# Kernel tuning notes

Hardware: AMD Instinct MI355X
Metric: run time of the kernel (lower is better)

## Reference

```python
import jax, jax.numpy as jnp
import numpy as np
import math

BS, S, D = 2, 2048, 2048
DOWN, UP, H, RD = 512, 1024, 16, 32
HD = D // H            # 128, used only in softmax scale
VD = UP // H           # 64 per-head value dim
CD = UP // H           # 64 per-head content q/k dim
SCALE = math.sqrt(HD) + math.sqrt(RD)


def _rope(x, head_dim):
    # x: [bs, heads, seq, head_dim]; standard rotate-half RoPE
    seq = x.shape[2]
    inv_freq = 1.0 / (10000.0 ** (jnp.arange(0, head_dim, 2, dtype=jnp.float32) / head_dim))
    freqs = jnp.arange(seq, dtype=jnp.float32)[:, None] * inv_freq[None, :]  # [S, hd/2]
    emb = jnp.concatenate([freqs, freqs], axis=-1)                            # [S, hd]
    cos = jnp.cos(emb)[None, None]
    sin = jnp.sin(emb)[None, None]
    x1, x2 = x[..., : head_dim // 2], x[..., head_dim // 2 :]
    rot = jnp.concatenate([-x2, x1], axis=-1)
    return x * cos + rot * sin


def setup_inputs() -> dict:
    key = jax.random.key(0)
    ks = jax.random.split(key, 10)
    sd = 0.02
    inp = {
        'h': jax.random.normal(ks[0], (BS, S, D), jnp.float32),
        'mask': jnp.tril(jnp.ones((1, 1, S, S), jnp.int32)),
        'Wdkv': jax.random.normal(ks[1], (DOWN, D), jnp.float32) * sd,
        'bdkv': jnp.zeros((DOWN,), jnp.float32),
        'Wuk': jax.random.normal(ks[2], (UP, DOWN), jnp.float32) * sd,
        'buk': jnp.zeros((UP,), jnp.float32),
        'Wuv': jax.random.normal(ks[3], (UP, DOWN), jnp.float32) * sd,
        'buv': jnp.zeros((UP,), jnp.float32),
        'Wdq': jax.random.normal(ks[4], (DOWN, D), jnp.float32) * sd,
        'bdq': jnp.zeros((DOWN,), jnp.float32),
        'Wuq': jax.random.normal(ks[5], (UP, DOWN), jnp.float32) * sd,
        'buq': jnp.zeros((UP,), jnp.float32),
        'Wqr': jax.random.normal(ks[6], (RD * H, DOWN), jnp.float32) * sd,
        'bqr': jnp.zeros((RD * H,), jnp.float32),
        'Wkr': jax.random.normal(ks[7], (RD, D), jnp.float32) * sd,
        'bkr': jnp.zeros((RD,), jnp.float32),
        'Wfc': jax.random.normal(ks[8], (D, H * VD), jnp.float32) * sd,
        'bfc': jnp.zeros((D,), jnp.float32),
    }
    return inp


def reference(h, mask, Wdkv, bdkv, Wuk, buk, Wuv, buv, Wdq, bdq, Wuq, buq,
              Wqr, bqr, Wkr, bkr, Wfc, bfc):
    bs, seq, _ = h.shape
    # low-rank KV path
    c_kv = h @ Wdkv.T + bdkv                                   # [bs,S,DOWN]
    k_c = (c_kv @ Wuk.T + buk).reshape(bs, seq, H, CD).transpose(0, 2, 1, 3)
    v_c = (c_kv @ Wuv.T + buv).reshape(bs, seq, H, VD).transpose(0, 2, 1, 3)
    # low-rank Q path
    c_q = h @ Wdq.T + bdq                                      # [bs,S,DOWN]
    q_c = (c_q @ Wuq.T + buq).reshape(bs, seq, H, CD).transpose(0, 2, 1, 3)
    # decoupled RoPE paths
    q_r = _rope((c_q @ Wqr.T + bqr).reshape(bs, seq, H, RD).transpose(0, 2, 1, 3), RD)
    k_r = _rope((h @ Wkr.T + bkr).reshape(bs, seq, 1, RD).transpose(0, 2, 1, 3), RD)
    k_r = jnp.broadcast_to(k_r, (bs, H, seq, RD))              # shared RoPE key across heads
    q = jnp.concatenate([q_c, q_r], axis=-1)                   # [bs,H,S,CD+RD]
    k = jnp.concatenate([k_c, k_r], axis=-1)
    scores = jnp.einsum('bhqd,bhkd->bhqk', q, k)
    # NB: original applies mask BEFORE dividing by scale
    scores = jnp.where(mask == 0, -1e9, scores)
    probs = jax.nn.softmax(scores / SCALE, axis=-1)
    out = jnp.einsum('bhqk,bhkd->bhqd', probs, v_c)            # [bs,H,S,VD]
    out = out.transpose(0, 2, 1, 3).reshape(bs, seq, H * VD)
    return out @ Wfc.T + bfc
```

## Files before the change

### kernel.cpp

```cpp
#include <hip/hip_runtime.h>
#include <hip/hip_bf16.h>
#include <math.h>

typedef unsigned short u16;
typedef __attribute__((ext_vector_type(8))) short bf16x8;
typedef __attribute__((ext_vector_type(4))) float f32x4;
typedef __attribute__((ext_vector_type(16))) float f32x16;

namespace {

constexpr int BS = 2;
constexpr int S = 2048;
constexpr int D = 2048;
constexpr int DOWN = 512;
constexpr int UP = 1024;
constexpr int H = 16;
constexpr int RD = 32;
constexpr int VD = 64;
constexpr int QKD = 96;
constexpr int M = BS * S;
constexpr int N1 = 1152;
constexpr int N2 = 2048;
constexpr int N3 = 1536;

__device__ __forceinline__ float b2f(u16 u) {
  unsigned int x = ((unsigned int)u) << 16;
  return __uint_as_float(x);
}
__device__ __forceinline__ u16 f2b(float f) {
  unsigned int u = __float_as_uint(f);
  u += 0x7fff + ((u >> 16) & 1);
  return (u16)(u >> 16);
}
__device__ __forceinline__ void store_out(float* p, float v) { *p = v; }
__device__ __forceinline__ void store_out(u16* p, float v) { *p = f2b(v); }

__device__ __forceinline__ void async16(const u16* g, u16* lds) {
  __builtin_amdgcn_global_load_lds(
      (const __attribute__((address_space(1))) unsigned int*)g,
      (__attribute__((address_space(3))) unsigned int*)lds, 16, 0, 0);
}

__device__ __forceinline__ float exp2_fast(float x) {
#if __has_builtin(__builtin_amdgcn_exp2f)
  return __builtin_amdgcn_exp2f(x);
#else
  float r;
  asm("v_exp_f32 %0, %1" : "=v"(r) : "v"(x));
  return r;
#endif
}

__device__ __forceinline__ unsigned pkbf(float a, float b) {
  union { __hip_bfloat162 h; unsigned u; } c;
  c.h = __float22bfloat162_rn(make_float2(a, b));
  return c.u;
}
__device__ __forceinline__ void plswap(unsigned& a, unsigned& b) {
  asm("v_permlane32_swap_b32 %0, %1" : "+v"(a), "+v"(b));
}

__device__ __forceinline__ f32x4 mfma32(bf16x8 a, bf16x8 b, f32x4 c) {
  return __builtin_amdgcn_mfma_f32_16x16x32_bf16(a, b, c, 0, 0, 0);
}
__device__ __forceinline__ f32x16 mfma3216(bf16x8 a, bf16x8 b, f32x16 c) {
  return __builtin_amdgcn_mfma_f32_32x32x16_bf16(a, b, c, 0, 0, 0);
}

__global__ __launch_bounds__(256) void prep_kernel(
    const float* __restrict__ h, const float* __restrict__ Wdkv,
    const float* __restrict__ Wdq, const float* __restrict__ Wkr,
    const float* __restrict__ Wuk, const float* __restrict__ Wuv,
    const float* __restrict__ Wuq, const float* __restrict__ Wqr,
    const float* __restrict__ Wfc, const float* __restrict__ bdkv,
    const float* __restrict__ bdq, const float* __restrict__ bkr,
    const float* __restrict__ buk, const float* __restrict__ buv,
    const float* __restrict__ buq, const float* __restrict__ bqr,
    u16* __restrict__ hb, u16* __restrict__ Wcat1, u16* __restrict__ Wcat2,
    u16* __restrict__ Wcat3, u16* __restrict__ Wfcb,
    float* __restrict__ bcat1, float* __restrict__ bcat2,
    float* __restrict__ bcat3, float* __restrict__ ct, float* __restrict__ st) {
  const long i = (long)blockIdx.x * 256 + threadIdx.x;
  if (i >= 3630240) return;
  if (i < 3620864) {
    const float* src; u16* dst; long off;
    if      (i < 2097152) { src = h;    dst = hb;              off = i; }
    else if (i < 2359296) { src = Wdkv; dst = Wcat1;           off = i - 2097152; }
    else if (i < 2621440) { src = Wdq;  dst = Wcat1 + 1048576; off = i - 2359296; }
    else if (i < 2637824) { src = Wkr;  dst = Wcat1 + 2097152; off = i - 2621440; }
    else if (i < 2768896) { src = Wuk;  dst = Wcat2;           off = i - 2637824; }
    else if (i < 2899968) { src = Wuv;  dst = Wcat2 + 524288;  off = i - 2768896; }
    else if (i < 3031040) { src = Wuq;  dst = Wcat3;           off = i - 2899968; }
    else if (i < 3096576) { src = Wqr;  dst = Wcat3 + 524288;  off = i - 3031040; }
    else                  { src = Wfc;  dst = Wfcb;            off = i - 3096576; }
    float4 v = ((const float4*)src)[off];
    ushort4 o;
    o.x = f2b(v.x); o.y = f2b(v.y); o.z = f2b(v.z); o.w = f2b(v.w);
    ((ushort4*)dst)[off] = o;
  } else if (i < 3622048) {
    long j0 = (i - 3620864) * 4;
#pragma unroll
    for (int e = 0; e < 4; ++e) {
      long j = j0 + e;
      if (j < N1) {
        float v = 0.f;
        if (j < 512) v = bdkv[j];
        else if (j < 1024) v = bdq[j - 512];
        else if (j < 1056) v = bkr[j - 1024];
        bcat1[j] = v;
      } else if (j < N1 + N2) {
        long jj = j - N1;
        bcat2[jj] = (jj < 1024) ? buk[jj] : buv[jj - 1024];
      } else {
        long jj = j - N1 - N2;
        bcat3[jj] = (jj < 1024) ? buq[jj] : bqr[jj - 1024];
      }
    }
  } else {
    long k0 = (i - 3622048) * 4;
#pragma unroll
    for (int e = 0; e < 4; ++e) {
      long k = k0 + e;
      int s = (int)(k >> 4), r = (int)(k & 15);
      float f = powf(10000.f, -(float)r / 16.f);
      float th = (float)s * f;
      ct[k] = cosf(th);
      st[k] = sinf(th);
    }
  }
}

template <int BN, typename OutT>
__device__ __forceinline__ void gemm_body(
    const u16* __restrict__ A, int lda, const u16* __restrict__ W, int ldw,
    const float* __restrict__ bias, OutT* __restrict__ C, int ldc, int K,
    int m0, int n0) {
  constexpr int NFR = BN / 32;
  __shared__ u16 As[128 * 32];
  __shared__ u16 Bs[BN * 32];
  const int t = threadIdx.x;
  const int lane = t & 63, wave = t >> 6;
  const int wm = (wave >> 1) * 64, wn = (wave & 1) * (BN / 2);
  const int lrow = lane & 15, lk = (lane >> 4) * 8;
  const int srow = lane >> 2, scol = (lane & 3) * 8;
  f32x4 acc[4][NFR] = {};
  for (int k0 = 0; k0 < K; k0 += 32) {
    __syncthreads();
    {
      int r = wave * 32 + srow;
      async16(A + (size_t)(m0 + r) * lda + k0 + scol, As + (wave * 32) * 32);
      async16(A + (size_t)(m0 + r + 16) * lda + k0 + scol,
              As + (wave * 32 + 16) * 32);
    }
    if (BN == 128) {
      int r = wave * 32 + srow;
      async16(W + (size_t)(n0 + r) * ldw + k0 + scol, Bs + (wave * 32) * 32);
      async16(W + (size_t)(n0 + r + 16) * ldw + k0 + scol,
              Bs + (wave * 32 + 16) * 32);
    } else {
      int r = wave * 16 + srow;
      async16(W + (size_t)(n0 + r) * ldw + k0 + scol, Bs + (wave * 16) * 32);
    }
    __syncthreads();
    bf16x8 af[4], bfr[NFR];
#pragma unroll
    for (int i = 0; i < 4; ++i)
      af[i] = *(const bf16x8*)(As + (wm + i * 16 + lrow) * 32 + lk);
#pragma unroll
    for (int i = 0; i < NFR; ++i)
      bfr[i] = *(const bf16x8*)(Bs + (wn + i * 16 + lrow) * 32 + lk);
#pragma unroll
    for (int mi = 0; mi < 4; ++mi)
#pragma unroll
      for (int ni = 0; ni < NFR; ++ni)
        acc[mi][ni] = mfma32(af[mi], bfr[ni], acc[mi][ni]);
  }
#pragma unroll
  for (int mi = 0; mi < 4; ++mi)
#pragma unroll
    for (int ni = 0; ni < NFR; ++ni)
#pragma unroll
      for (int r = 0; r < 4; ++r) {
        int m = m0 + wm + mi * 16 + (lane >> 4) * 4 + r;
        int n = n0 + wn + ni * 16 + lrow;
        store_out(C + (size_t)m * ldc + n, acc[mi][ni][r] + bias[n]);
      }
}

template <int BN, typename OutT>
__global__ __launch_bounds__(256) void gemm_bt_mfma(
    const u16* __restrict__ A, int lda, const u16* __restrict__ W, int ldw,
    const float* __restrict__ bias, OutT* __restrict__ C, int ldc, int K) {
  gemm_body<BN, OutT>(A, lda, W, ldw, bias, C, ldc, K,
                      blockIdx.x * 128, blockIdx.y * BN);
}

__global__ __launch_bounds__(256) void gemm_up_fused(
    const u16* __restrict__ C1v, const u16* __restrict__ Wcat2,
    const u16* __restrict__ Wcat3, const float* __restrict__ bcat2,
    const float* __restrict__ bcat3, u16* __restrict__ C2,
    u16* __restrict__ C3) {
  const int by = blockIdx.y;
  const u16* A;
  const u16* W;
  const float* bias;
  u16* C;
  int ldc, n0;
  if (by < 16) {
    A = C1v; W = Wcat2; bias = bcat2; C = C2; ldc = N2; n0 = by * 128;
  } else {
    A = C1v + DOWN; W = Wcat3; bias = bcat3; C = C3; ldc = N3;
    n0 = (by - 16) * 128;
  }
  gemm_body<128, u16>(A, N1, W, DOWN, bias, C, ldc, DOWN,
                      blockIdx.x * 128, n0);
}

__global__ __launch_bounds__(256) void transpose_v_kernel(
    const u16* __restrict__ in, int ld_in, u16* __restrict__ VtB) {
  __shared__ u16 tile[64][72];
  const int m0 = blockIdx.x * 64;
  const int h = blockIdx.y;
  const int r = threadIdx.x >> 2, c0 = (threadIdx.x & 3) * 16;
  *(bf16x8*)(&tile[r][c0]) =
      *(const bf16x8*)(in + (size_t)(m0 + r) * ld_in + h * VD + c0);
  *(bf16x8*)(&tile[r][c0 + 8]) =
      *(const bf16x8*)(in + (size_t)(m0 + r) * ld_in + h * VD + c0 + 8);
  __syncthreads();
  bf16x8 o0, o1;
#pragma unroll
  for (int j = 0; j < 8; ++j) {
    o0[j] = (short)tile[c0 + j][r];
    o1[j] = (short)tile[c0 + 8 + j][r];
  }
  const int b = m0 / S, sb = m0 % S;
  size_t dst = ((size_t)(b * H + h) * 64 + ((sb + c0) >> 5)) * 2048 +
               (size_t)r * 32 + ((sb + c0) & 31);
  *(bf16x8*)(VtB + dst) = o0;
  *(bf16x8*)(VtB + dst + 8) = o1;
}

__global__ __launch_bounds__(192) void pack_q_kernel(
    const u16* __restrict__ qc, const u16* __restrict__ qr,
    const float* __restrict__ ct, const float* __restrict__ st,
    u16* __restrict__ Qp) {
  const int t = threadIdx.x;
  const int sub = (t >= 96) ? 1 : 0;
  const int d = t - sub * 96;
  const int s = blockIdx.x * 2 + sub, h = blockIdx.y, b = blockIdx.z;
  const float sc = 1.44269504088896f / (sqrtf(128.f) + sqrtf(32.f));
  float val;
  if (d < 64) {
    val = b2f(qc[(size_t)(b * S + s) * N3 + h * VD + d]);
  } else {
    int r = d - 64;
    const u16* qrow = qr + (size_t)(b * S + s) * N3 + h * RD;
    float x = b2f(qrow[r]), xp = b2f(qrow[r ^ 16]);
    float c = ct[s * 16 + (r & 15)], sn = st[s * 16 + (r & 15)];
    val = (r < 16) ? (x * c - xp * sn) : (x * c + xp * sn);
  }
  Qp[((size_t)(b * H + h) * S + s) * QKD + d] = f2b(val * sc);
}

__global__ __launch_bounds__(192) void pack_k_kernel(
    const u16* __restrict__ kc,
    const u16* __restrict__ kr,
    const float* __restrict__ ct, const float* __restrict__ st,
    u16* __restrict__ Kp) {
  const int t = threadIdx.x;
  const int sub = (t >= 96) ? 1 : 0;
  const int d = t - sub * 96;
  const int s = blockIdx.x * 2 + sub, h = blockIdx.y, b = blockIdx.z;
  float val;
  if (d < 64) {
    val = b2f(kc[(size_t)(b * S + s) * N2 + h * VD + d]);
  } else {
    int r = d - 64;
    const u16* krow = kr + (size_t)(b * S + s) * N1;
    float x = b2f(krow[r]), xp = b2f(krow[r ^ 16]);
    float c = ct[s * 16 + (r & 15)], sn = st[s * 16 + (r & 15)];
    val = (r < 16) ? (x * c - xp * sn) : (x * c + xp * sn);
  }
  Kp[((size_t)(b * H + h) * S + s) * QKD + d] = f2b(val);
}

__global__ __launch_bounds__(256, 3) void attn_mfma(
    const u16* __restrict__ Qp, const u16* __restrict__ Kp,
    const u16* __restrict__ Vt, u16* __restrict__ attnb) {
  const int t = threadIdx.x, wave = t >> 6, lane = t & 63;
  const int l31 = lane & 31, hw = lane >> 5;
  const int bh = blockIdx.x & 31;
  const int b = bh >> 4, h = bh & 15;
  const int tile = 63 - (blockIdx.x >> 5);
  const int q0w = tile * 32;
  const size_t hbo = (size_t)bh * S;

  __shared__ float red[3][64][33];

  bf16x8 qf[6];
  {
    const u16* qrow = Qp + (hbo + q0w + l31) * QKD + hw * 8;
#pragma unroll
    for (int c = 0; c < 6; ++c) qf[c] = *(const bf16x8*)(qrow + c * 16);
  }
  f32x16 O0 = {0,0,0,0,0,0,0,0,0,0,0,0,0,0,0,0};
  f32x16 O1 = {0,0,0,0,0,0,0,0,0,0,0,0,0,0,0,0};
  float lsum = 0.f;
  const int q_abs = q0w + l31;
  const u16* vbase = Vt + (size_t)bh * 64 * 2048 + l31 * 32 + 8 * hw;

  bf16x8 kf[6];
  {
    const u16* kb = Kp + (hbo + wave * 32 + l31) * QKD + hw * 8;
#pragma unroll
    for (int c = 0; c < 6; ++c) kf[c] = *(const bf16x8*)(kb + c * 16);
  }

  for (int m = wave; m <= tile; m += 4) {
    const int k0 = m * 32;
    const u16* vb = vbase + (size_t)m * 2048;
    bf16x8 vf00 = *(const bf16x8*)(vb);
    bf16x8 vf01 = *(const bf16x8*)(vb + 16);
    bf16x8 vf10 = *(const bf16x8*)(vb + 1024);
    bf16x8 vf11 = *(const bf16x8*)(vb + 1024 + 16);
    f32x16 sa = {0,0,0,0,0,0,0,0,0,0,0,0,0,0,0,0};
    f32x16 sb = {0,0,0,0,0,0,0,0,0,0,0,0,0,0,0,0};
    sa = mfma3216(kf[0], qf[0], sa);
    sb = mfma3216(kf[1], qf[1], sb);
    sa = mfma3216(kf[2], qf[2], sa);
    sb = mfma3216(kf[3], qf[3], sb);
    sa = mfma3216(kf[4], qf[4], sa);
    sb = mfma3216(kf[5], qf[5], sb);
    if (m + 4 <= tile) {
      const u16* kb = Kp + (hbo + (size_t)(m + 4) * 32 + l31) * QKD + hw * 8;
#pragma unroll
      for (int c = 0; c < 6; ++c) kf[c] = *(const bf16x8*)(kb + c * 16);
    }
    float e[16];
    if (m == tile) {
#pragma unroll
      for (int r = 0; r < 16; ++r) {
        int key_abs = k0 + (r & 3) + 8 * (r >> 2) + 4 * hw;
        float v = exp2_fast(sa[r] + sb[r]);
        e[r] = (key_abs <= q_abs) ? v : 0.f;
      }
    } else {
#pragma unroll
      for (int r = 0; r < 16; ++r) e[r] = exp2_fast(sa[r] + sb[r]);
    }
    {
      float p0 = (e[0] + e[1]) + (e[2] + e[3]);
      float p1 = (e[4] + e[5]) + (e[6] + e[7]);
      float p2 = (e[8] + e[9]) + (e[10] + e[11]);
      float p3 = (e[12] + e[13]) + (e[14] + e[15]);
      lsum += (p0 + p1) + (p2 + p3);
    }
    unsigned w0 = pkbf(e[0], e[1]),   w1 = pkbf(e[2], e[3]);
    unsigned w2 = pkbf(e[4], e[5]),   w3 = pkbf(e[6], e[7]);
    unsigned w4 = pkbf(e[8], e[9]),   w5 = pkbf(e[10], e[11]);
    unsigned w6 = pkbf(e[12], e[13]), w7 = pkbf(e[14], e[15]);
    plswap(w0, w2); plswap(w1, w3); plswap(w4, w6); plswap(w5, w7);
    union { unsigned u[4]; bf16x8 v; } ua, ub;
    ua.u[0] = w0; ua.u[1] = w1; ua.u[2] = w2; ua.u[3] = w3;
    ub.u[0] = w4; ub.u[1] = w5; ub.u[2] = w6; ub.u[3] = w7;
    O0 = mfma3216(ua.v, vf00, O0);
    O1 = mfma3216(ua.v, vf10, O1);
    O0 = mfma3216(ub.v, vf01, O0);
    O1 = mfma3216(ub.v, vf11, O1);
  }

  if (wave > 0) {
#pragma unroll
    for (int r = 0; r < 16; ++r) {
      red[wave - 1][lane][r] = O0[r];
      red[wave - 1][lane][16 + r] = O1[r];
    }
    red[wave - 1][lane][32] = lsum;
  }
  __syncthreads();
  if (wave == 0) {
#pragma unroll
    for (int w = 0; w < 3; ++w) {
#pragma unroll
      for (int r = 0; r < 16; ++r) {
        O0[r] += red[w][lane][r];
        O1[r] += red[w][lane][16 + r];
      }
      lsum += red[w][lane][32];
    }
    float tot = lsum + __shfl_xor(lsum, 32);
    u16* ob = attnb + (size_t)b * S * UP + h * VD;
#pragma unroll
    for (int r = 0; r < 16; ++r) {
      int rowq = (r & 3) + 8 * (r >> 2) + 4 * hw;
      float linv = 1.f / __shfl(tot, rowq);
      size_t rowoff = (size_t)(q0w + rowq) * UP;
      ob[rowoff + l31] = f2b(O0[r] * linv);
      ob[rowoff + 32 + l31] = f2b(O1[r] * linv);
    }
  }
}

}

extern "C" void kernel_launch(void* const* d_in, const int* in_sizes, int n_in,
                              void* d_out, int out_size, void* d_ws, size_t ws_size,
                              hipStream_t stream) {
  const float* h    = (const float*)d_in[0];
  const float* Wdkv = (const float*)d_in[2];
  const float* bdkv = (const float*)d_in[3];
  const float* Wuk  = (const float*)d_in[4];
  const float* buk  = (const float*)d_in[5];
  const float* Wuv  = (const float*)d_in[6];
  const float* buv  = (const float*)d_in[7];
  const float* Wdq  = (const float*)d_in[8];
  const float* bdq  = (const float*)d_in[9];
  const float* Wuq  = (const float*)d_in[10];
  const float* buq  = (const float*)d_in[11];
  const float* Wqr  = (const float*)d_in[12];
  const float* bqr  = (const float*)d_in[13];
  const float* Wkr  = (const float*)d_in[14];
  const float* bkr  = (const float*)d_in[15];
  const float* Wfc  = (const float*)d_in[16];
  const float* bfc  = (const float*)d_in[17];
  float* out = (float*)d_out;

  u16* p = (u16*)d_ws;
  u16* hb    = p; p += (size_t)M * D;
  u16* Wcat1 = p; p += (size_t)N1 * D;
  u16* Wcat2 = p; p += (size_t)N2 * DOWN;
  u16* Wcat3 = p; p += (size_t)N3 * DOWN;
  u16* Wfcb  = p; p += (size_t)D * UP;
  u16* C1    = p; p += (size_t)M * N1;
  u16* C2    = p; p += (size_t)M * N2;
  u16* C3    = p; p += (size_t)M * N3;
  u16* Qp    = p; p += 6291456;
  u16* Kp    = p; p += 6291456;
  u16* Vt    = p; p += (size_t)UP * M;
  float* bcat1 = (float*)p; p += 2 * N1;
  float* bcat2 = (float*)p; p += 2 * N2;
  float* bcat3 = (float*)p; p += 2 * N3;
  float* ct = (float*)p; p += 2 * S * 16;
  float* st = (float*)p; p += 2 * S * 16;
  u16* attnb = C1;

  prep_kernel<<<dim3(14181), 256, 0, stream>>>(
      h, Wdkv, Wdq, Wkr, Wuk, Wuv, Wuq, Wqr, Wfc,
      bdkv, bdq, bkr, buk, buv, buq, bqr,
      hb, Wcat1, Wcat2, Wcat3, Wfcb, bcat1, bcat2, bcat3, ct, st);

  gemm_bt_mfma<64, u16><<<dim3(M / 128, N1 / 64), 256, 0, stream>>>(
      hb, D, Wcat1, D, bcat1, C1, N1, D);
  gemm_up_fused<<<dim3(M / 128, 28), 256, 0, stream>>>(
      C1, Wcat2, Wcat3, bcat2, bcat3, C2, C3);

  pack_q_kernel<<<dim3(S / 2, H, BS), 192, 0, stream>>>(
      C3, C3 + UP, ct, st, Qp);
  pack_k_kernel<<<dim3(S / 2, H, BS), 192, 0, stream>>>(
      C2, C1 + 2 * DOWN, ct, st, Kp);
  transpose_v_kernel<<<dim3(M / 64, UP / 64), 256, 0, stream>>>(
      C2 + UP, N2, Vt);

  attn_mfma<<<dim3(2048), 256, 0, stream>>>(Qp, Kp, Vt, attnb);

  gemm_bt_mfma<64, float><<<dim3(M / 128, D / 64), 256, 0, stream>>>(
      attnb, UP, Wfcb, UP, bfc, out, D, UP);
}
```

Before: 318.3 us.

## Pair causal attention tiles per block, double-buffer K/V loads, widen GEMM tiles

The attention kernel now handles two query tiles per block (tile 63-tp and tp), so every block does a similar amount of causal work. The grid shrinks to 1024 blocks and the launch-bound occupancy drops from 3 to 2. K and V fragments are prefetched into ping-pong register buffers so the V loads also overlap compute. Separately, the first projection GEMM and the output GEMM switch to 128-wide N tiles, which halves their grid size. This raises register pressure and reduces the number of blocks, which risks lower occupancy and tail effects.

```diff
diff --git a/kernel.cpp b/kernel.cpp
--- a/kernel.cpp
+++ b/kernel.cpp
@@ -284,120 +284,152 @@
   Kp[((size_t)(b * H + h) * S + s) * QKD + d] = f2b(val);
 }
 
-__global__ __launch_bounds__(256, 3) void attn_mfma(
+__global__ __launch_bounds__(256, 2) void attn_mfma(
     const u16* __restrict__ Qp, const u16* __restrict__ Kp,
     const u16* __restrict__ Vt, u16* __restrict__ attnb) {
   const int t = threadIdx.x, wave = t >> 6, lane = t & 63;
   const int l31 = lane & 31, hw = lane >> 5;
   const int bh = blockIdx.x & 31;
   const int b = bh >> 4, h = bh & 15;
-  const int tile = 63 - (blockIdx.x >> 5);
-  const int q0w = tile * 32;
+  const int tp = blockIdx.x >> 5;
   const size_t hbo = (size_t)bh * S;
+  const u16* vbase = Vt + (size_t)bh * 64 * 2048 + l31 * 32 + 8 * hw;
 
   __shared__ float red[3][64][33];
 
-  bf16x8 qf[6];
-  {
-    const u16* qrow = Qp + (hbo + q0w + l31) * QKD + hw * 8;
-#pragma unroll
-    for (int c = 0; c < 6; ++c) qf[c] = *(const bf16x8*)(qrow + c * 16);
-  }
-  f32x16 O0 = {0,0,0,0,0,0,0,0,0,0,0,0,0,0,0,0};
-  f32x16 O1 = {0,0,0,0,0,0,0,0,0,0,0,0,0,0,0,0};
-  float lsum = 0.f;
-  const int q_abs = q0w + l31;
-  const u16* vbase = Vt + (size_t)bh * 64 * 2048 + l31 * 32 + 8 * hw;
-
-  bf16x8 kf[6];
-  {
-    const u16* kb = Kp + (hbo + wave * 32 + l31) * QKD + hw * 8;
-#pragma unroll
-    for (int c = 0; c < 6; ++c) kf[c] = *(const bf16x8*)(kb + c * 16);
-  }
-
-  for (int m = wave; m <= tile; m += 4) {
-    const int k0 = m * 32;
-    const u16* vb = vbase + (size_t)m * 2048;
-    bf16x8 vf00 = *(const bf16x8*)(vb);
-    bf16x8 vf01 = *(const bf16x8*)(vb + 16);
-    bf16x8 vf10 = *(const bf16x8*)(vb + 1024);
-    bf16x8 vf11 = *(const bf16x8*)(vb + 1024 + 16);
-    f32x16 sa = {0,0,0,0,0,0,0,0,0,0,0,0,0,0,0,0};
-    f32x16 sb = {0,0,0,0,0,0,0,0,0,0,0,0,0,0,0,0};
-    sa = mfma3216(kf[0], qf[0], sa);
-    sb = mfma3216(kf[1], qf[1], sb);
-    sa = mfma3216(kf[2], qf[2], sa);
-    sb = mfma3216(kf[3], qf[3], sb);
-    sa = mfma3216(kf[4], qf[4], sa);
-    sb = mfma3216(kf[5], qf[5], sb);
-    if (m + 4 <= tile) {
-      const u16* kb = Kp + (hbo + (size_t)(m + 4) * 32 + l31) * QKD + hw * 8;
-#pragma unroll
-      for (int c = 0; c < 6; ++c) kf[c] = *(const bf16x8*)(kb + c * 16);
-    }
-    float e[16];
-    if (m == tile) {
+#pragma unroll 1
+  for (int pass = 0; pass < 2; ++pass) {
+    const int tile = pass ? tp : 63 - tp;
+    const int q0w = tile * 32;
+    const int q_abs = q0w + l31;
+
+    bf16x8 qf[6];
+    {
+      const u16* qrow = Qp + (hbo + q0w + l31) * QKD + hw * 8;
+#pragma unroll
+      for (int c = 0; c < 6; ++c) qf[c] = *(const bf16x8*)(qrow + c * 16);
+    }
+    f32x16 O0 = {0,0,0,0,0,0,0,0,0,0,0,0,0,0,0,0};
+    f32x16 O1 = {0,0,0,0,0,0,0,0,0,0,0,0,0,0,0,0};
+    float lsum = 0.f;
+
+    auto step = [&](const bf16x8* kf, const bf16x8* vf, int m) {
+      f32x16 sa = {0,0,0,0,0,0,0,0,0,0,0,0,0,0,0,0};
+      f32x16 sb = {0,0,0,0,0,0,0,0,0,0,0,0,0,0,0,0};
+      sa = mfma3216(kf[0], qf[0], sa);
+      sb = mfma3216(kf[1], qf[1], sb);
+      sa = mfma3216(kf[2], qf[2], sa);
+      sb = mfma3216(kf[3], qf[3], sb);
+      sa = mfma3216(kf[4], qf[4], sa);
+      sb = mfma3216(kf[5], qf[5], sb);
+      float e[16];
+      if (m == tile) {
+        const int k0 = m * 32;
+#pragma unroll
+        for (int r = 0; r < 16; ++r) {
+          int key_abs = k0 + (r & 3) + 8 * (r >> 2) + 4 * hw;
+          float v = exp2_fast(sa[r] + sb[r]);
+          e[r] = (key_abs <= q_abs) ? v : 0.f;
+        }
+      } else {
+#pragma unroll
+        for (int r = 0; r < 16; ++r) e[r] = exp2_fast(sa[r] + sb[r]);
+      }
+      {
+        float p0 = (e[0] + e[1]) + (e[2] + e[3]);
+        float p1 = (e[4] + e[5]) + (e[6] + e[7]);
+        float p2 = (e[8] + e[9]) + (e[10] + e[11]);
+        float p3 = (e[12] + e[13]) + (e[14] + e[15]);
+        lsum += (p0 + p1) + (p2 + p3);
+      }
+      unsigned w0 = pkbf(e[0], e[1]),   w1 = pkbf(e[2], e[3]);
+      unsigned w2 = pkbf(e[4], e[5]),   w3 = pkbf(e[6], e[7]);
+      unsigned w4 = pkbf(e[8], e[9]),   w5 = pkbf(e[10], e[11]);
+      unsigned w6 = pkbf(e[12], e[13]), w7 = pkbf(e[14], e[15]);
+      plswap(w0, w2); plswap(w1, w3); plswap(w4, w6); plswap(w5, w7);
+      union { unsigned u[4]; bf16x8 v; } ua, ub;
+      ua.u[0] = w0; ua.u[1] = w1; ua.u[2] = w2; ua.u[3] = w3;
+      ub.u[0] = w4; ub.u[1] = w5; ub.u[2] = w6; ub.u[3] = w7;
+      O0 = mfma3216(ua.v, vf[0], O0);
+      O1 = mfma3216(ua.v, vf[2], O1);
+      O0 = mfma3216(ub.v, vf[1], O0);
+      O1 = mfma3216(ub.v, vf[3], O1);
+    };
+
+    if (tile >= wave) {
+      bf16x8 kfE[6], kfO[6], vfE[4], vfO[4];
+      int m = wave;
+      {
+        const u16* kb = Kp + (hbo + (size_t)m * 32 + l31) * QKD + hw * 8;
+#pragma unroll
+        for (int c = 0; c < 6; ++c) kfE[c] = *(const bf16x8*)(kb + c * 16);
+        const u16* vb = vbase + (size_t)m * 2048;
+        vfE[0] = *(const bf16x8*)(vb);
+        vfE[1] = *(const bf16x8*)(vb + 16);
+        vfE[2] = *(const bf16x8*)(vb + 1024);
+        vfE[3] = *(const bf16x8*)(vb + 1024 + 16);
+      }
+      while (true) {
+        if (m + 4 <= tile) {
+          const u16* kb = Kp + (hbo + (size_t)(m + 4) * 32 + l31) * QKD + hw * 8;
+#pragma unroll
+          for (int c = 0; c < 6; ++c) kfO[c] = *(const bf16x8*)(kb + c * 16);
+          const u16* vb = vbase + (size_t)(m + 4) * 2048;
+          vfO[0] = *(const bf16x8*)(vb);
+          vfO[1] = *(const bf16x8*)(vb + 16);
+          vfO[2] = *(const bf16x8*)(vb + 1024);
+          vfO[3] = *(const bf16x8*)(vb + 1024 + 16);
+        }
+        step(kfE, vfE, m);
+        m += 4;
+        if (m > tile) break;
+        if (m + 4 <= tile) {
+          const u16* kb = Kp + (hbo + (size_t)(m + 4) * 32 + l31) * QKD + hw * 8;
+#pragma unroll
+          for (int c = 0; c < 6; ++c) kfE[c] = *(const bf16x8*)(kb + c * 16);
+          const u16* vb = vbase + (size_t)(m + 4) * 2048;
+          vfE[0] = *(const bf16x8*)(vb);
+          vfE[1] = *(const bf16x8*)(vb + 16);
+          vfE[2] = *(const bf16x8*)(vb + 1024);
+          vfE[3] = *(const bf16x8*)(vb + 1024 + 16);
+        }
+        step(kfO, vfO, m);
+        m += 4;
+        if (m > tile) break;
+      }
+    }
+
+    if (wave > 0) {
 #pragma unroll
       for (int r = 0; r < 16; ++r) {
-        int key_abs = k0 + (r & 3) + 8 * (r >> 2) + 4 * hw;
-        float v = exp2_fast(sa[r] + sb[r]);
-        e[r] = (key_abs <= q_abs) ? v : 0.f;
-      }
-    } else {
-#pragma unroll
-      for (int r = 0; r < 16; ++r) e[r] = exp2_fast(sa[r] + sb[r]);
-    }
-    {
-      float p0 = (e[0] + e[1]) + (e[2] + e[3]);
-      float p1 = (e[4] + e[5]) + (e[6] + e[7]);
-      float p2 = (e[8] + e[9]) + (e[10] + e[11]);
-      float p3 = (e[12] + e[13]) + (e[14] + e[15]);
-      lsum += (p0 + p1) + (p2 + p3);
-    }
-    unsigned w0 = pkbf(e[0], e[1]),   w1 = pkbf(e[2], e[3]);
-    unsigned w2 = pkbf(e[4], e[5]),   w3 = pkbf(e[6], e[7]);
-    unsigned w4 = pkbf(e[8], e[9]),   w5 = pkbf(e[10], e[11]);
-    unsigned w6 = pkbf(e[12], e[13]), w7 = pkbf(e[14], e[15]);
-    plswap(w0, w2); plswap(w1, w3); plswap(w4, w6); plswap(w5, w7);
-    union { unsigned u[4]; bf16x8 v; } ua, ub;
-    ua.u[0] = w0; ua.u[1] = w1; ua.u[2] = w2; ua.u[3] = w3;
-    ub.u[0] = w4; ub.u[1] = w5; ub.u[2] = w6; ub.u[3] = w7;
-    O0 = mfma3216(ua.v, vf00, O0);
-    O1 = mfma3216(ua.v, vf10, O1);
-    O0 = mfma3216(ub.v, vf01, O0);
-    O1 = mfma3216(ub.v, vf11, O1);
-  }
-
-  if (wave > 0) {
-#pragma unroll
-    for (int r = 0; r < 16; ++r) {
-      red[wave - 1][lane][r] = O0[r];
-      red[wave - 1][lane][16 + r] = O1[r];
-    }
-    red[wave - 1][lane][32] = lsum;
-  }
-  __syncthreads();
-  if (wave == 0) {
-#pragma unroll
-    for (int w = 0; w < 3; ++w) {
+        red[wave - 1][lane][r] = O0[r];
+        red[wave - 1][lane][16 + r] = O1[r];
+      }
+      red[wave - 1][lane][32] = lsum;
+    }
+    __syncthreads();
+    if (wave == 0) {
+#pragma unroll
+      for (int w = 0; w < 3; ++w) {
+#pragma unroll
+        for (int r = 0; r < 16; ++r) {
+          O0[r] += red[w][lane][r];
+          O1[r] += red[w][lane][16 + r];
+        }
+        lsum += red[w][lane][32];
+      }
+      float tot = lsum + __shfl_xor(lsum, 32);
+      u16* ob = attnb + (size_t)b * S * UP + h * VD;
 #pragma unroll
       for (int r = 0; r < 16; ++r) {
-        O0[r] += red[w][lane][r];
-        O1[r] += red[w][lane][16 + r];
-      }
-      lsum += red[w][lane][32];
-    }
-    float tot = lsum + __shfl_xor(lsum, 32);
-    u16* ob = attnb + (size_t)b * S * UP + h * VD;
-#pragma unroll
-    for (int r = 0; r < 16; ++r) {
-      int rowq = (r & 3) + 8 * (r >> 2) + 4 * hw;
-      float linv = 1.f / __shfl(tot, rowq);
-      size_t rowoff = (size_t)(q0w + rowq) * UP;
-      ob[rowoff + l31] = f2b(O0[r] * linv);
-      ob[rowoff + 32 + l31] = f2b(O1[r] * linv);
-    }
+        int rowq = (r & 3) + 8 * (r >> 2) + 4 * hw;
+        float linv = 1.f / __shfl(tot, rowq);
+        size_t rowoff = (size_t)(q0w + rowq) * UP;
+        ob[rowoff + l31] = f2b(O0[r] * linv);
+        ob[rowoff + 32 + l31] = f2b(O1[r] * linv);
+      }
+    }
+    __syncthreads();
   }
 }
 
@@ -449,7 +481,7 @@
       bdkv, bdq, bkr, buk, buv, buq, bqr,
       hb, Wcat1, Wcat2, Wcat3, Wfcb, bcat1, bcat2, bcat3, ct, st);
 
-  gemm_bt_mfma<64, u16><<<dim3(M / 128, N1 / 64), 256, 0, stream>>>(
+  gemm_bt_mfma<128, u16><<<dim3(M / 128, N1 / 128), 256, 0, stream>>>(
       hb, D, Wcat1, D, bcat1, C1, N1, D);
   gemm_up_fused<<<dim3(M / 128, 28), 256, 0, stream>>>(
       C1, Wcat2, Wcat3, bcat2, bcat3, C2, C3);
@@ -461,8 +493,8 @@
   transpose_v_kernel<<<dim3(M / 64, UP / 64), 256, 0, stream>>>(
       C2 + UP, N2, Vt);
 
-  attn_mfma<<<dim3(2048), 256, 0, stream>>>(Qp, Kp, Vt, attnb);
-
-  gemm_bt_mfma<64, float><<<dim3(M / 128, D / 64), 256, 0, stream>>>(
+  attn_mfma<<<dim3(1024), 256, 0, stream>>>(Qp, Kp, Vt, attnb);
+
+  gemm_bt_mfma<128, float><<<dim3(M / 128, D / 128), 256, 0, stream>>>(
       attnb, UP, Wfcb, UP, bfc, out, D, UP);
 }
```

Measured after the change: 325.6 us. 1.02x slower.

## Restructure attention to share LDS-staged K/V tiles across waves; widen GEMM tiles

Applied to the files above, without the earlier changes.

The attention kernel previously split one 32-query tile's key loop across four waves and combined their partial results through shared memory. Now each block covers four consecutive query tiles, one per wave. K and V chunks are staged into double-buffered LDS with async copies and shared by all waves, and the cross-wave reduction is removed. This cuts redundant global K/V loads, at the cost of a barrier every iteration, load imbalance across waves near the causal diagonal, and fewer blocks (512). The two plain GEMM launches also move from 64 to 128 N-tiles, which halves their grid sizes.

```diff
diff --git a/kernel.cpp b/kernel.cpp
--- a/kernel.cpp
+++ b/kernel.cpp
@@ -284,18 +284,26 @@
   Kp[((size_t)(b * H + h) * S + s) * QKD + d] = f2b(val);
 }
 
-__global__ __launch_bounds__(256, 3) void attn_mfma(
+__global__ __launch_bounds__(256, 2) void attn_mfma(
     const u16* __restrict__ Qp, const u16* __restrict__ Kp,
     const u16* __restrict__ Vt, u16* __restrict__ attnb) {
   const int t = threadIdx.x, wave = t >> 6, lane = t & 63;
   const int l31 = lane & 31, hw = lane >> 5;
   const int bh = blockIdx.x & 31;
   const int b = bh >> 4, h = bh & 15;
-  const int tile = 63 - (blockIdx.x >> 5);
-  const int q0w = tile * 32;
+  const int qq = 15 - (int)(blockIdx.x >> 5);
+  const int mtop = qq * 4 + 3;
+  const int tw = qq * 4 + wave;
+  const int q0w = tw * 32;
   const size_t hbo = (size_t)bh * S;
 
-  __shared__ float red[3][64][33];
+  __shared__ u16 KsB[2][3072];
+  __shared__ u16 VsB[2][2048];
+
+  const u16* kpb = Kp + hbo * QKD;
+  const int ksrc = l31 * QKD + hw * 8;
+  const u16* vtb = Vt + (size_t)bh * 64 * 2048;
+  const int vsrc = lane * 32;
 
   bf16x8 qf[6];
   {
@@ -307,97 +315,89 @@
   f32x16 O1 = {0,0,0,0,0,0,0,0,0,0,0,0,0,0,0,0};
   float lsum = 0.f;
   const int q_abs = q0w + l31;
-  const u16* vbase = Vt + (size_t)bh * 64 * 2048 + l31 * 32 + 8 * hw;
-
-  bf16x8 kf[6];
-  {
-    const u16* kb = Kp + (hbo + wave * 32 + l31) * QKD + hw * 8;
-#pragma unroll
-    for (int c = 0; c < 6; ++c) kf[c] = *(const bf16x8*)(kb + c * 16);
-  }
-
-  for (int m = wave; m <= tile; m += 4) {
-    const int k0 = m * 32;
-    const u16* vb = vbase + (size_t)m * 2048;
-    bf16x8 vf00 = *(const bf16x8*)(vb);
-    bf16x8 vf01 = *(const bf16x8*)(vb + 16);
-    bf16x8 vf10 = *(const bf16x8*)(vb + 1024);
-    bf16x8 vf11 = *(const bf16x8*)(vb + 1024 + 16);
-    f32x16 sa = {0,0,0,0,0,0,0,0,0,0,0,0,0,0,0,0};
-    f32x16 sb = {0,0,0,0,0,0,0,0,0,0,0,0,0,0,0,0};
-    sa = mfma3216(kf[0], qf[0], sa);
-    sb = mfma3216(kf[1], qf[1], sb);
-    sa = mfma3216(kf[2], qf[2], sa);
-    sb = mfma3216(kf[3], qf[3], sb);
-    sa = mfma3216(kf[4], qf[4], sa);
-    sb = mfma3216(kf[5], qf[5], sb);
-    if (m + 4 <= tile) {
-      const u16* kb = Kp + (hbo + (size_t)(m + 4) * 32 + l31) * QKD + hw * 8;
-#pragma unroll
-      for (int c = 0; c < 6; ++c) kf[c] = *(const bf16x8*)(kb + c * 16);
-    }
-    float e[16];
-    if (m == tile) {
-#pragma unroll
-      for (int r = 0; r < 16; ++r) {
-        int key_abs = k0 + (r & 3) + 8 * (r >> 2) + 4 * hw;
-        float v = exp2_fast(sa[r] + sb[r]);
-        e[r] = (key_abs <= q_abs) ? v : 0.f;
+
+  auto stage = [&](int buf, int m) {
+    const u16* kr = kpb + (size_t)m * 32 * QKD + ksrc;
+    const u16* vr = vtb + (size_t)m * 2048 + vsrc;
+    u16* ks = &KsB[buf][0];
+    u16* vs = &VsB[buf][0];
+    for (int idx = wave; idx < 10; idx += 4) {
+      if (idx < 6) {
+        async16(kr + idx * 16, ks + idx * 512);
+      } else {
+        int j = idx - 6;
+        async16(vr + (j >> 1) * 16 + (j & 1) * 8, vs + j * 512);
       }
-    } else {
-#pragma unroll
-      for (int r = 0; r < 16; ++r) e[r] = exp2_fast(sa[r] + sb[r]);
-    }
-    {
-      float p0 = (e[0] + e[1]) + (e[2] + e[3]);
-      float p1 = (e[4] + e[5]) + (e[6] + e[7]);
-      float p2 = (e[8] + e[9]) + (e[10] + e[11]);
-      float p3 = (e[12] + e[13]) + (e[14] + e[15]);
-      lsum += (p0 + p1) + (p2 + p3);
-    }
-    unsigned w0 = pkbf(e[0], e[1]),   w1 = pkbf(e[2], e[3]);
-    unsigned w2 = pkbf(e[4], e[5]),   w3 = pkbf(e[6], e[7]);
-    unsigned w4 = pkbf(e[8], e[9]),   w5 = pkbf(e[10], e[11]);
-    unsigned w6 = pkbf(e[12], e[13]), w7 = pkbf(e[14], e[15]);
-    plswap(w0, w2); plswap(w1, w3); plswap(w4, w6); plswap(w5, w7);
-    union { unsigned u[4]; bf16x8 v; } ua, ub;
-    ua.u[0] = w0; ua.u[1] = w1; ua.u[2] = w2; ua.u[3] = w3;
-    ub.u[0] = w4; ub.u[1] = w5; ub.u[2] = w6; ub.u[3] = w7;
-    O0 = mfma3216(ua.v, vf00, O0);
-    O1 = mfma3216(ua.v, vf10, O1);
-    O0 = mfma3216(ub.v, vf01, O0);
-    O1 = mfma3216(ub.v, vf11, O1);
-  }
-
-  if (wave > 0) {
-#pragma unroll
-    for (int r = 0; r < 16; ++r) {
-      red[wave - 1][lane][r] = O0[r];
-      red[wave - 1][lane][16 + r] = O1[r];
-    }
-    red[wave - 1][lane][32] = lsum;
-  }
+    }
+  };
+
+  stage(0, 0);
   __syncthreads();
-  if (wave == 0) {
-#pragma unroll
-    for (int w = 0; w < 3; ++w) {
-#pragma unroll
-      for (int r = 0; r < 16; ++r) {
-        O0[r] += red[w][lane][r];
-        O1[r] += red[w][lane][16 + r];
+  for (int m = 0; m <= mtop; ++m) {
+    if (m < mtop) stage((m + 1) & 1, m + 1);
+    if (m <= tw) {
+      const u16* ks = &KsB[m & 1][lane * 8];
+      const u16* vs = &VsB[m & 1][hw * 512 + l31 * 8];
+      bf16x8 kf[6];
+#pragma unroll
+      for (int c = 0; c < 6; ++c) kf[c] = *(const bf16x8*)(ks + c * 512);
+      f32x16 sa = {0,0,0,0,0,0,0,0,0,0,0,0,0,0,0,0};
+      f32x16 sb = {0,0,0,0,0,0,0,0,0,0,0,0,0,0,0,0};
+      sa = mfma3216(kf[0], qf[0], sa);
+      sb = mfma3216(kf[1], qf[1], sb);
+      sa = mfma3216(kf[2], qf[2], sa);
+      sb = mfma3216(kf[3], qf[3], sb);
+      sa = mfma3216(kf[4], qf[4], sa);
+      sb = mfma3216(kf[5], qf[5], sb);
+      float e[16];
+      if (m == tw) {
+        const int k0 = m * 32;
+#pragma unroll
+        for (int r = 0; r < 16; ++r) {
+          int key_abs = k0 + (r & 3) + 8 * (r >> 2) + 4 * hw;
+          float v = exp2_fast(sa[r] + sb[r]);
+          e[r] = (key_abs <= q_abs) ? v : 0.f;
+        }
+      } else {
+#pragma unroll
+        for (int r = 0; r < 16; ++r) e[r] = exp2_fast(sa[r] + sb[r]);
       }
-      lsum += red[w][lane][32];
-    }
-    float tot = lsum + __shfl_xor(lsum, 32);
-    u16* ob = attnb + (size_t)b * S * UP + h * VD;
-#pragma unroll
-    for (int r = 0; r < 16; ++r) {
-      int rowq = (r & 3) + 8 * (r >> 2) + 4 * hw;
-      float linv = 1.f / __shfl(tot, rowq);
-      size_t rowoff = (size_t)(q0w + rowq) * UP;
-      ob[rowoff + l31] = f2b(O0[r] * linv);
-      ob[rowoff + 32 + l31] = f2b(O1[r] * linv);
-    }
+      {
+        float p0 = (e[0] + e[1]) + (e[2] + e[3]);
+        float p1 = (e[4] + e[5]) + (e[6] + e[7]);
+        float p2 = (e[8] + e[9]) + (e[10] + e[11]);
+        float p3 = (e[12] + e[13]) + (e[14] + e[15]);
+        lsum += (p0 + p1) + (p2 + p3);
+      }
+      unsigned w0 = pkbf(e[0], e[1]),   w1 = pkbf(e[2], e[3]);
+      unsigned w2 = pkbf(e[4], e[5]),   w3 = pkbf(e[6], e[7]);
+      unsigned w4 = pkbf(e[8], e[9]),   w5 = pkbf(e[10], e[11]);
+      unsigned w6 = pkbf(e[12], e[13]), w7 = pkbf(e[14], e[15]);
+      plswap(w0, w2); plswap(w1, w3); plswap(w4, w6); plswap(w5, w7);
+      union { unsigned u[4]; bf16x8 v; } ua, ub;
+      ua.u[0] = w0; ua.u[1] = w1; ua.u[2] = w2; ua.u[3] = w3;
+      ub.u[0] = w4; ub.u[1] = w5; ub.u[2] = w6; ub.u[3] = w7;
+      bf16x8 vf00 = *(const bf16x8*)(vs);
+      bf16x8 vf10 = *(const bf16x8*)(vs + 256);
+      bf16x8 vf01 = *(const bf16x8*)(vs + 1024);
+      bf16x8 vf11 = *(const bf16x8*)(vs + 1280);
+      O0 = mfma3216(ua.v, vf00, O0);
+      O1 = mfma3216(ua.v, vf10, O1);
+      O0 = mfma3216(ub.v, vf01, O0);
+      O1 = mfma3216(ub.v, vf11, O1);
+    }
+    __syncthreads();
+  }
+
+  float tot = lsum + __shfl_xor(lsum, 32);
+  u16* ob = attnb + (size_t)b * S * UP + h * VD;
+#pragma unroll
+  for (int r = 0; r < 16; ++r) {
+    int rowq = (r & 3) + 8 * (r >> 2) + 4 * hw;
+    float linv = 1.f / __shfl(tot, rowq);
+    size_t rowoff = (size_t)(q0w + rowq) * UP;
+    ob[rowoff + l31] = f2b(O0[r] * linv);
+    ob[rowoff + 32 + l31] = f2b(O1[r] * linv);
   }
 }
 
@@ -449,7 +449,7 @@
       bdkv, bdq, bkr, buk, buv, buq, bqr,
       hb, Wcat1, Wcat2, Wcat3, Wfcb, bcat1, bcat2, bcat3, ct, st);
 
-  gemm_bt_mfma<64, u16><<<dim3(M / 128, N1 / 64), 256, 0, stream>>>(
+  gemm_bt_mfma<128, u16><<<dim3(M / 128, N1 / 128), 256, 0, stream>>>(
       hb, D, Wcat1, D, bcat1, C1, N1, D);
   gemm_up_fused<<<dim3(M / 128, 28), 256, 0, stream>>>(
       C1, Wcat2, Wcat3, bcat2, bcat3, C2, C3);
@@ -461,8 +461,8 @@
   transpose_v_kernel<<<dim3(M / 64, UP / 64), 256, 0, stream>>>(
       C2 + UP, N2, Vt);
 
-  attn_mfma<<<dim3(2048), 256, 0, stream>>>(Qp, Kp, Vt, attnb);
-
-  gemm_bt_mfma<64, float><<<dim3(M / 128, D / 64), 256, 0, stream>>>(
+  attn_mfma<<<dim3(512), 256, 0, stream>>>(Qp, Kp, Vt, attnb);
+
+  gemm_bt_mfma<128, float><<<dim3(M / 128, D / 128), 256, 0, stream>>>(
       attnb, UP, Wfcb, UP, bfc, out, D, UP);
 }
```

Result: slower. 334.9 us (+5.2%).

## Double-buffer V loads in attention, remap blocks per XCD, widen GEMM tiles

Applied to the files above, without the earlier changes.

The attention loop now prefetches the next V tile into alternating register buffers alongside the K prefetch, so the loads overlap the current tile's MFMA and softmax work. Blocks are remapped so that each XCD handles a fixed group of four (batch, head) pairs, which should improve L2 reuse of K and V. The first and last GEMMs switch from 64-wide to 128-wide N tiles, halving their grid sizes. The added register buffers raise register pressure and could reduce occupancy, and the wider GEMM tiles leave fewer blocks to spread across the CUs.

```diff
diff --git a/kernel.cpp b/kernel.cpp
--- a/kernel.cpp
+++ b/kernel.cpp
@@ -289,9 +289,10 @@
     const u16* __restrict__ Vt, u16* __restrict__ attnb) {
   const int t = threadIdx.x, wave = t >> 6, lane = t & 63;
   const int l31 = lane & 31, hw = lane >> 5;
-  const int bh = blockIdx.x & 31;
+  const int xcd = (int)(blockIdx.x & 7), sub = (int)(blockIdx.x >> 3);
+  const int bh = xcd * 4 + (sub & 3);
+  const int tile = 63 - (sub >> 2);
   const int b = bh >> 4, h = bh & 15;
-  const int tile = 63 - (blockIdx.x >> 5);
   const int q0w = tile * 32;
   const size_t hbo = (size_t)bh * S;
 
@@ -308,36 +309,21 @@
   float lsum = 0.f;
   const int q_abs = q0w + l31;
   const u16* vbase = Vt + (size_t)bh * 64 * 2048 + l31 * 32 + 8 * hw;
-
-  bf16x8 kf[6];
-  {
-    const u16* kb = Kp + (hbo + wave * 32 + l31) * QKD + hw * 8;
-#pragma unroll
-    for (int c = 0; c < 6; ++c) kf[c] = *(const bf16x8*)(kb + c * 16);
-  }
-
-  for (int m = wave; m <= tile; m += 4) {
-    const int k0 = m * 32;
-    const u16* vb = vbase + (size_t)m * 2048;
-    bf16x8 vf00 = *(const bf16x8*)(vb);
-    bf16x8 vf01 = *(const bf16x8*)(vb + 16);
-    bf16x8 vf10 = *(const bf16x8*)(vb + 1024);
-    bf16x8 vf11 = *(const bf16x8*)(vb + 1024 + 16);
-    f32x16 sa = {0,0,0,0,0,0,0,0,0,0,0,0,0,0,0,0};
-    f32x16 sb = {0,0,0,0,0,0,0,0,0,0,0,0,0,0,0,0};
+  const u16* kpb = Kp + hbo * QKD;
+
+  auto qk_part1 = [&](bf16x8* kf, f32x16& sa, f32x16& sb) {
     sa = mfma3216(kf[0], qf[0], sa);
     sb = mfma3216(kf[1], qf[1], sb);
     sa = mfma3216(kf[2], qf[2], sa);
     sb = mfma3216(kf[3], qf[3], sb);
     sa = mfma3216(kf[4], qf[4], sa);
     sb = mfma3216(kf[5], qf[5], sb);
-    if (m + 4 <= tile) {
-      const u16* kb = Kp + (hbo + (size_t)(m + 4) * 32 + l31) * QKD + hw * 8;
-#pragma unroll
-      for (int c = 0; c < 6; ++c) kf[c] = *(const bf16x8*)(kb + c * 16);
-    }
+  };
+  auto finish = [&](const f32x16& sa, const f32x16& sb, const bf16x8* vf,
+                    int m) {
     float e[16];
     if (m == tile) {
+      const int k0 = m * 32;
 #pragma unroll
       for (int r = 0; r < 16; ++r) {
         int key_abs = k0 + (r & 3) + 8 * (r >> 2) + 4 * hw;
@@ -363,10 +349,51 @@
     union { unsigned u[4]; bf16x8 v; } ua, ub;
     ua.u[0] = w0; ua.u[1] = w1; ua.u[2] = w2; ua.u[3] = w3;
     ub.u[0] = w4; ub.u[1] = w5; ub.u[2] = w6; ub.u[3] = w7;
-    O0 = mfma3216(ua.v, vf00, O0);
-    O1 = mfma3216(ua.v, vf10, O1);
-    O0 = mfma3216(ub.v, vf01, O0);
-    O1 = mfma3216(ub.v, vf11, O1);
+    O0 = mfma3216(ua.v, vf[0], O0);
+    O1 = mfma3216(ua.v, vf[2], O1);
+    O0 = mfma3216(ub.v, vf[1], O0);
+    O1 = mfma3216(ub.v, vf[3], O1);
+  };
+  auto loadK = [&](int m, bf16x8* kf) {
+    const u16* kb = kpb + (size_t)(m * 32 + l31) * QKD + hw * 8;
+#pragma unroll
+    for (int c = 0; c < 6; ++c) kf[c] = *(const bf16x8*)(kb + c * 16);
+  };
+  auto loadV = [&](int m, bf16x8* vf) {
+    const u16* vb = vbase + (size_t)m * 2048;
+    vf[0] = *(const bf16x8*)(vb);
+    vf[1] = *(const bf16x8*)(vb + 16);
+    vf[2] = *(const bf16x8*)(vb + 1024);
+    vf[3] = *(const bf16x8*)(vb + 1024 + 16);
+  };
+
+  if (tile >= wave) {
+    bf16x8 kf[6], vfE[4], vfO[4];
+    int m = wave;
+    loadK(m, kf);
+    loadV(m, vfE);
+    while (true) {
+      {
+        if (m + 4 <= tile) loadV(m + 4, vfO);
+        f32x16 sa = {0,0,0,0,0,0,0,0,0,0,0,0,0,0,0,0};
+        f32x16 sb = {0,0,0,0,0,0,0,0,0,0,0,0,0,0,0,0};
+        qk_part1(kf, sa, sb);
+        if (m + 4 <= tile) loadK(m + 4, kf);
+        finish(sa, sb, vfE, m);
+      }
+      m += 4;
+      if (m > tile) break;
+      {
+        if (m + 4 <= tile) loadV(m + 4, vfE);
+        f32x16 sa = {0,0,0,0,0,0,0,0,0,0,0,0,0,0,0,0};
+        f32x16 sb = {0,0,0,0,0,0,0,0,0,0,0,0,0,0,0,0};
+        qk_part1(kf, sa, sb);
+        if (m + 4 <= tile) loadK(m + 4, kf);
+        finish(sa, sb, vfO, m);
+      }
+      m += 4;
+      if (m > tile) break;
+    }
   }
 
   if (wave > 0) {
@@ -449,7 +476,7 @@
       bdkv, bdq, bkr, buk, buv, buq, bqr,
       hb, Wcat1, Wcat2, Wcat3, Wfcb, bcat1, bcat2, bcat3, ct, st);
 
-  gemm_bt_mfma<64, u16><<<dim3(M / 128, N1 / 64), 256, 0, stream>>>(
+  gemm_bt_mfma<128, u16><<<dim3(M / 128, N1 / 128), 256, 0, stream>>>(
       hb, D, Wcat1, D, bcat1, C1, N1, D);
   gemm_up_fused<<<dim3(M / 128, 28), 256, 0, stream>>>(
       C1, Wcat2, Wcat3, bcat2, bcat3, C2, C3);
@@ -463,6 +490,6 @@
 
   attn_mfma<<<dim3(2048), 256, 0, stream>>>(Qp, Kp, Vt, attnb);
 
-  gemm_bt_mfma<64, float><<<dim3(M / 128, D / 64), 256, 0, stream>>>(
+  gemm_bt_mfma<128, float><<<dim3(M / 128, D / 128), 256, 0, stream>>>(
       attnb, UP, Wfcb, UP, bfc, out, D, UP);
 }
```

Result: no change. 318.9 us (+0.2%).
